# Kernel tuning notes

Measured on AMD Instinct MI355X. Metric: run time of the kernel, lower is better.

## Reference

```python
import jax, jax.numpy as jnp
import numpy as np

NUM_HEADS = 16


def _mhsa(x, Wq, Wk, Wv, Wo):
    B, S, D = x.shape
    H = NUM_HEADS
    dk = D // H
    # Linear applies weight [out, in]: y = x @ W.T
    Q = jnp.einsum('bsd,ed->bse', x, Wq).reshape(B, S, H, dk).transpose(0, 2, 1, 3)
    K = jnp.einsum('bsd,ed->bse', x, Wk).reshape(B, S, H, dk).transpose(0, 2, 1, 3)
    V = jnp.einsum('bsd,ed->bse', x, Wv).reshape(B, S, H, dk).transpose(0, 2, 1, 3)
    scores = jnp.einsum('bhqd,bhkd->bhqk', Q, K) / jnp.sqrt(jnp.asarray(dk, x.dtype))
    causal = jnp.tril(jnp.ones((S, S), dtype=bool))  # True = keep
    scores = jnp.where(causal, scores, jnp.asarray(-jnp.inf, x.dtype))
    attn = jax.nn.softmax(scores, axis=-1)
    out = jnp.einsum('bhqk,bhkd->bhqd', attn, V)  # [B,H,S,dk]
    out = out.transpose(0, 2, 1, 3).reshape(B, S, D)
    return jnp.einsum('bsd,ed->bse', out, Wo)


def setup_inputs() -> dict:
    key = jax.random.key(0)
    ks = jax.random.split(key, 5)
    B, S, D = 4, 2048, 1024
    std = 2.0 / (D + D) ** 0.5
    return {
        'x': jax.random.normal(ks[0], (B, S, D), dtype=jnp.float32),
        'Wq': jax.random.normal(ks[1], (D, D), dtype=jnp.float32) * std,
        'Wk': jax.random.normal(ks[2], (D, D), dtype=jnp.float32) * std,
        'Wv': jax.random.normal(ks[3], (D, D), dtype=jnp.float32) * std,
        'Wo': jax.random.normal(ks[4], (D, D), dtype=jnp.float32) * std,
    }


def reference(x, Wq, Wk, Wv, Wo):
    return _mhsa(x, Wq, Wk, Wv, Wo)
```

## Files before the change

### kernel.cpp

```cpp
#include <hip/hip_runtime.h>
#include <hip/hip_bf16.h>
#include <stdint.h>

typedef __attribute__((ext_vector_type(8))) short short8;
typedef __attribute__((ext_vector_type(4))) float f32x4;

static __device__ __forceinline__ void gload_lds16(const void* g, void* l) {
  __builtin_amdgcn_global_load_lds((const __attribute__((address_space(1))) void*)g,
                                   (__attribute__((address_space(3))) void*)l,
                                   16, 0, 0);
}

static __device__ __forceinline__ unsigned short f2bf(float f) {
  union { __hip_bfloat16 h; unsigned short s; } u;
  u.h = __float2bfloat16(f);
  return u.s;
}

__global__ void cast_all(const float* __restrict__ x, const float* __restrict__ Wq,
                         const float* __restrict__ Wk, const float* __restrict__ Wv,
                         const float* __restrict__ Wo,
                         unsigned short* __restrict__ xb, unsigned short* __restrict__ Wqb,
                         unsigned short* __restrict__ Wkb, unsigned short* __restrict__ Wvb,
                         unsigned short* __restrict__ Wob) {
  const int i = blockIdx.x * 256 + threadIdx.x;
  const float* src;
  unsigned short* dst;
  int off;
  if (i < 2097152) {
    src = x; dst = xb; off = i;
  } else {
    const int j = i - 2097152;
    const int wsel = j >> 18;
    off = j & 262143;
    src = wsel == 0 ? Wq : wsel == 1 ? Wk : wsel == 2 ? Wv : Wo;
    dst = wsel == 0 ? Wqb : wsel == 1 ? Wkb : wsel == 2 ? Wvb : Wob;
  }
  float4 v = reinterpret_cast<const float4*>(src)[off];
  ushort4 o;
  o.x = f2bf(v.x); o.y = f2bf(v.y); o.z = f2bf(v.z); o.w = f2bf(v.w);
  reinterpret_cast<ushort4*>(dst)[off] = o;
}

template <typename OutT>
static __device__ __forceinline__ void gemm_tile(const unsigned short* __restrict__ A,
                                                 const unsigned short* __restrict__ B,
                                                 OutT* __restrict__ C,
                                                 int brow, int bcol, int ldc,
                                                 short* sA0, short* sA1,
                                                 short* sB0, short* sB1) {
  const int t = threadIdx.x;
  const int w = t >> 6, l = t & 63, lg = l >> 4, lr = l & 15;
  const int wr = w >> 1, wc = w & 1;
  short* sAb[2] = {sA0, sA1};
  short* sBb[2] = {sB0, sB1};

  f32x4 acc[4][4] = {};

  auto stage = [&](int buf, int kt) {
#pragma unroll
    for (int r = 0; r < 2; ++r) {
      const int byteoff = t * 16 + r * 4096;
      const int row = byteoff >> 6, inrow = byteoff & 63;
      gload_lds16((const char*)A + ((size_t)(brow + row) * 1024 + kt) * 2 + inrow,
                  (char*)sAb[buf] + byteoff);
      gload_lds16((const char*)B + ((size_t)(bcol + row) * 1024 + kt) * 2 + inrow,
                  (char*)sBb[buf] + byteoff);
    }
  };

  stage(0, 0);
  __syncthreads();
  int cur = 0;

  for (int kti = 0; kti < 32; ++kti) {
    if (kti + 1 < 32) stage(cur ^ 1, (kti + 1) << 5);

    short8 af[4], bfr[4];
#pragma unroll
    for (int m = 0; m < 4; ++m)
      af[m] = *reinterpret_cast<const short8*>(sAb[cur] + (wr * 64 + m * 16 + lr) * 32 + lg * 8);
#pragma unroll
    for (int n = 0; n < 4; ++n)
      bfr[n] = *reinterpret_cast<const short8*>(sBb[cur] + (wc * 64 + n * 16 + lr) * 32 + lg * 8);
#pragma unroll
    for (int m = 0; m < 4; ++m)
#pragma unroll
      for (int n = 0; n < 4; ++n)
        acc[m][n] = __builtin_amdgcn_mfma_f32_16x16x32_bf16(af[m], bfr[n], acc[m][n], 0, 0, 0);

    __syncthreads();
    cur ^= 1;
  }

#pragma unroll
  for (int m = 0; m < 4; ++m) {
#pragma unroll
    for (int n = 0; n < 4; ++n) {
#pragma unroll
      for (int j = 0; j < 4; ++j) {
        const int rr = brow + wr * 64 + m * 16 + lg * 4 + j;
        const int cc = bcol + wc * 64 + n * 16 + lr;
        if constexpr (sizeof(OutT) == 2) {
          C[(size_t)rr * ldc + cc] = (OutT)f2bf(acc[m][n][j]);
        } else {
          C[(size_t)rr * ldc + cc] = acc[m][n][j];
        }
      }
    }
  }
}

__global__ __launch_bounds__(256) void gemm_qkv(const unsigned short* __restrict__ xb,
                                                const unsigned short* __restrict__ Wqb,
                                                const unsigned short* __restrict__ Wkb,
                                                const unsigned short* __restrict__ Wvb,
                                                unsigned short* __restrict__ Qb,
                                                unsigned short* __restrict__ Kb,
                                                unsigned short* __restrict__ Vt) {
  __shared__ short sA[2][4096];
  __shared__ short sB[2][4096];
  const int i = blockIdx.x;
  const int lid = (i & 7) * 192 + (i >> 3);
  const int z = lid >> 9, r = lid & 511;

  const unsigned short *A, *B;
  unsigned short* C;
  int brow, bcol, ldc;
  if (z == 2) {
    A = Wvb; B = xb; C = Vt;
    brow = (r & 7) << 7; bcol = (r >> 3) << 7; ldc = 8192;
  } else {
    A = xb; B = z ? Wkb : Wqb; C = z ? Kb : Qb;
    brow = (r >> 3) << 7; bcol = (r & 7) << 7; ldc = 1024;
  }
  gemm_tile<unsigned short>(A, B, C, brow, bcol, ldc, sA[0], sA[1], sB[0], sB[1]);
}

__global__ __launch_bounds__(256) void gemm_out(const unsigned short* __restrict__ AO,
                                                const unsigned short* __restrict__ Wob,
                                                float* __restrict__ out) {
  __shared__ short sA[2][4096];
  __shared__ short sB[2][4096];
  const int i = blockIdx.x;
  const int lid = (i & 7) * 64 + (i >> 3);
  gemm_tile<float>(AO, Wob, out, (lid >> 3) << 7, (lid & 7) << 7, 1024,
                   sA[0], sA[1], sB[0], sB[1]);
}

__global__ __launch_bounds__(256) void attn_kernel(const unsigned short* __restrict__ Qg,
                                                   const unsigned short* __restrict__ Kg,
                                                   const unsigned short* __restrict__ Vtg,
                                                   unsigned short* __restrict__ AO) {
  const int S = 2048, D = 1024, SN = 8192;
  const int i = blockIdx.x;
  const int lid = (i & 7) * 128 + (i >> 3);
  const int qp = lid & 15;
  const int bh = lid >> 4;
  const int b = bh >> 4, h = bh & 15;
  const int t = threadIdx.x;
  const int w = t >> 6, l = t & 63, lg = l >> 4, lr = l & 15;

  __shared__ short sK[2][64 * 64];
  __shared__ short sV[2][64 * 64];
  __shared__ short sP[4 * 16 * 64];

  int sboff[2], slin[2], srow[2];
#pragma unroll
  for (int r = 0; r < 2; ++r) {
    sboff[r] = t * 16 + r * 4096;
    srow[r] = sboff[r] >> 7;
    slin[r] = (sboff[r] & 127) ^ ((srow[r] & 7) << 4);
  }
  const char* Kbase = (const char*)Kg + ((size_t)(b * S) * D + h * 64) * 2;
  const char* Vbase = (const char*)Vtg + ((size_t)(h * 64) * SN + (size_t)b * S) * 2;

  auto stage = [&](int buf, int kvt) {
    const size_t kv0 = (size_t)kvt * 64;
#pragma unroll
    for (int r = 0; r < 2; ++r) {
      gload_lds16(Kbase + (kv0 + srow[r]) * 2048 + slin[r], (char*)sK[buf] + sboff[r]);
      gload_lds16(Vbase + (size_t)srow[r] * 16384 + kv0 * 2 + slin[r],
                  (char*)sV[buf] + sboff[r]);
    }
  };

  const float SCL = 0.125f * 1.44269504089f;
  int cur = 0;
  stage(0, 0);

#pragma unroll 1
  for (int half = 0; half < 2; ++half) {
    const int qt = half ? (31 - qp) : qp;
    const int nkv = qt + 1;

    short8 qf[2];
    {
      const unsigned short* qbase =
          Qg + (size_t)(b * S + qt * 64 + w * 16 + lr) * D + h * 64;
      qf[0] = *reinterpret_cast<const short8*>(qbase + lg * 8);
      qf[1] = *reinterpret_cast<const short8*>(qbase + 32 + lg * 8);
    }

    f32x4 o[4] = {};
    float m = -INFINITY, lsum = 0.f;

    __syncthreads();

    for (int kvt = 0; kvt < nkv; ++kvt) {
      if (kvt + 1 < nkv) stage(cur ^ 1, kvt + 1);

      const char* sKc = (const char*)sK[cur];
      const char* sVc = (const char*)sV[cur];

      f32x4 sc[4] = {};
      __builtin_amdgcn_s_setprio(1);
#pragma unroll
      for (int n = 0; n < 4; ++n) {
#pragma unroll
        for (int kk = 0; kk < 2; ++kk) {
          const int row = n * 16 + lr;
          const short8 kf = *reinterpret_cast<const short8*>(
              sKc + (row << 7) + ((kk * 64 + lg * 16) ^ ((row & 7) << 4)));
          sc[n] = __builtin_amdgcn_mfma_f32_16x16x32_bf16(kf, qf[kk], sc[n], 0, 0, 0);
        }
      }
      __builtin_amdgcn_s_setprio(0);

      float p[4][4];
      const bool diag = (kvt == qt);
      const int ql = w * 16 + lr;
#pragma unroll
      for (int n = 0; n < 4; ++n) {
#pragma unroll
        for (int r = 0; r < 4; ++r) {
          float v = sc[n][r] * SCL;
          if (diag && (n * 16 + lg * 4 + r) > ql) v = -INFINITY;
          p[n][r] = v;
        }
      }

      float mx = p[0][0];
#pragma unroll
      for (int n = 0; n < 4; ++n)
#pragma unroll
        for (int r = 0; r < 4; ++r) mx = fmaxf(mx, p[n][r]);
      mx = fmaxf(mx, __shfl_xor(mx, 16));
      mx = fmaxf(mx, __shfl_xor(mx, 32));
      if (!__all(mx <= m + 8.0f)) {
        const float mnew = fmaxf(m, mx);
        const float alpha = __builtin_amdgcn_exp2f(m - mnew);
        m = mnew;
        lsum *= alpha;
#pragma unroll
        for (int dn = 0; dn < 4; ++dn) o[dn] *= alpha;
      }

      float s = 0.f;
#pragma unroll
      for (int n = 0; n < 4; ++n) {
#pragma unroll
        for (int r = 0; r < 4; ++r) {
          const float e = __builtin_amdgcn_exp2f(p[n][r] - m);
          p[n][r] = e;
          s += e;
        }
      }
      s += __shfl_xor(s, 16);
      s += __shfl_xor(s, 32);
      lsum += s;

#pragma unroll
      for (int n = 0; n < 4; ++n) {
        ushort4 pk;
        pk.x = f2bf(p[n][0]); pk.y = f2bf(p[n][1]);
        pk.z = f2bf(p[n][2]); pk.w = f2bf(p[n][3]);
        *reinterpret_cast<ushort4*>(
            (char*)sP + (w << 11) + (lr << 7) + ((n * 32 + lg * 8) ^ ((lr & 7) << 4))) = pk;
      }

      __builtin_amdgcn_s_setprio(1);
#pragma unroll
      for (int kk = 0; kk < 2; ++kk) {
        const short8 pa = *reinterpret_cast<const short8*>(
            (const char*)sP + (w << 11) + (lr << 7) +
            ((kk * 64 + lg * 16) ^ ((lr & 7) << 4)));
#pragma unroll
        for (int dn = 0; dn < 4; ++dn) {
          const int vrow = dn * 16 + lr;
          const short8 vb = *reinterpret_cast<const short8*>(
              sVc + (vrow << 7) + ((kk * 64 + lg * 16) ^ ((vrow & 7) << 4)));
          o[dn] = __builtin_amdgcn_mfma_f32_16x16x32_bf16(vb, pa, o[dn], 0, 0, 0);
        }
      }
      __builtin_amdgcn_s_setprio(0);

      __syncthreads();
      cur ^= 1;
    }

    if (half == 0) stage(cur, 0);

    const float inv = 1.f / lsum;
    unsigned short* orow = AO + (size_t)(b * S + qt * 64 + w * 16 + lr) * D + h * 64;
#pragma unroll
    for (int dn = 0; dn < 4; ++dn) {
      ushort4 ov;
      ov.x = f2bf(o[dn][0] * inv); ov.y = f2bf(o[dn][1] * inv);
      ov.z = f2bf(o[dn][2] * inv); ov.w = f2bf(o[dn][3] * inv);
      *reinterpret_cast<ushort4*>(orow + dn * 16 + lg * 4) = ov;
    }
  }
}

extern "C" void kernel_launch(void* const* d_in, const int* in_sizes, int n_in,
                              void* d_out, int out_size, void* d_ws, size_t ws_size,
                              hipStream_t stream) {
  const float* x  = (const float*)d_in[0];
  const float* Wq = (const float*)d_in[1];
  const float* Wk = (const float*)d_in[2];
  const float* Wv = (const float*)d_in[3];
  const float* Wo = (const float*)d_in[4];
  float* out = (float*)d_out;

  char* ws = (char*)d_ws;
  unsigned short* xb  = (unsigned short*)(ws);
  unsigned short* Wqb = (unsigned short*)(ws + 16777216);
  unsigned short* Wkb = (unsigned short*)(ws + 18874368);
  unsigned short* Wvb = (unsigned short*)(ws + 20971520);
  unsigned short* Wob = (unsigned short*)(ws + 23068672);
  unsigned short* Qb  = (unsigned short*)(ws + 25165824);
  unsigned short* Kb  = (unsigned short*)(ws + 41943040);
  unsigned short* Vt  = (unsigned short*)(ws + 58720256);
  unsigned short* AO  = (unsigned short*)(ws + 75497472);

  cast_all<<<12288, 256, 0, stream>>>(x, Wq, Wk, Wv, Wo, xb, Wqb, Wkb, Wvb, Wob);
  gemm_qkv<<<1536, 256, 0, stream>>>(xb, Wqb, Wkb, Wvb, Qb, Kb, Vt);
  attn_kernel<<<1024, 256, 0, stream>>>(Qb, Kb, Vt, AO);
  gemm_out<<<512, 256, 0, stream>>>(AO, Wob, out);
}
```

Measured before the change: 286.1 us.

## Triple-buffer GEMM and attention loads with single barrier and swizzled LDS

GEMM tiles switch from double to triple LDS buffering, prefetch two stages ahead, and use a single waitcnt+barrier per iteration in place of two syncthreads. The GEMM LDS rows are XOR-swizzled to cut bank conflicts on the fragment reads. The attention kernel merges its two causal query-tile halves into one flat 33-step loop, so K/V prefetch runs across the half boundary without a pipeline drain. The cost is more LDS per block, which may lower occupancy, and reliance on hand-written vmcnt counts being correct.

```diff
diff --git a/kernel.cpp b/kernel.cpp
--- a/kernel.cpp
+++ b/kernel.cpp
@@ -16,6 +16,9 @@
   u.h = __float2bfloat16(f);
   return u.s;
 }
+
+#define WAIT4_BARRIER() asm volatile("s_waitcnt vmcnt(4) lgkmcnt(0)\n\ts_barrier" ::: "memory")
+#define WAIT0_BARRIER() asm volatile("s_waitcnt vmcnt(0) lgkmcnt(0)\n\ts_barrier" ::: "memory")
 
 __global__ void cast_all(const float* __restrict__ x, const float* __restrict__ Wq,
                          const float* __restrict__ Wk, const float* __restrict__ Wv,
@@ -47,13 +50,10 @@
                                                  const unsigned short* __restrict__ B,
                                                  OutT* __restrict__ C,
                                                  int brow, int bcol, int ldc,
-                                                 short* sA0, short* sA1,
-                                                 short* sB0, short* sB1) {
+                                                 short* sA, short* sB) {
   const int t = threadIdx.x;
   const int w = t >> 6, l = t & 63, lg = l >> 4, lr = l & 15;
   const int wr = w >> 1, wc = w & 1;
-  short* sAb[2] = {sA0, sA1};
-  short* sBb[2] = {sB0, sB1};
 
   f32x4 acc[4][4] = {};
 
@@ -61,36 +61,51 @@
 #pragma unroll
     for (int r = 0; r < 2; ++r) {
       const int byteoff = t * 16 + r * 4096;
-      const int row = byteoff >> 6, inrow = byteoff & 63;
+      const int row = byteoff >> 6;
+      const int inrow = (byteoff & 63) ^ (((row >> 1) & 3) << 4);
       gload_lds16((const char*)A + ((size_t)(brow + row) * 1024 + kt) * 2 + inrow,
-                  (char*)sAb[buf] + byteoff);
+                  (char*)(sA + buf * 4096) + byteoff);
       gload_lds16((const char*)B + ((size_t)(bcol + row) * 1024 + kt) * 2 + inrow,
-                  (char*)sBb[buf] + byteoff);
+                  (char*)(sB + buf * 4096) + byteoff);
     }
   };
 
   stage(0, 0);
-  __syncthreads();
+  stage(1, 32);
   int cur = 0;
 
   for (int kti = 0; kti < 32; ++kti) {
-    if (kti + 1 < 32) stage(cur ^ 1, (kti + 1) << 5);
+    if (kti < 31) WAIT4_BARRIER();
+    else         WAIT0_BARRIER();
+    if (kti + 2 < 32) {
+      int b2 = cur + 2; if (b2 >= 3) b2 -= 3;
+      stage(b2, (kti + 2) << 5);
+    }
+    const char* sAc = (const char*)(sA + cur * 4096);
+    const char* sBc = (const char*)(sB + cur * 4096);
 
     short8 af[4], bfr[4];
 #pragma unroll
-    for (int m = 0; m < 4; ++m)
-      af[m] = *reinterpret_cast<const short8*>(sAb[cur] + (wr * 64 + m * 16 + lr) * 32 + lg * 8);
-#pragma unroll
-    for (int n = 0; n < 4; ++n)
-      bfr[n] = *reinterpret_cast<const short8*>(sBb[cur] + (wc * 64 + n * 16 + lr) * 32 + lg * 8);
+    for (int m = 0; m < 4; ++m) {
+      const int arow = wr * 64 + m * 16 + lr;
+      af[m] = *reinterpret_cast<const short8*>(
+          sAc + arow * 64 + ((lg * 16) ^ (((arow >> 1) & 3) << 4)));
+    }
+#pragma unroll
+    for (int n = 0; n < 4; ++n) {
+      const int brw = wc * 64 + n * 16 + lr;
+      bfr[n] = *reinterpret_cast<const short8*>(
+          sBc + brw * 64 + ((lg * 16) ^ (((brw >> 1) & 3) << 4)));
+    }
+    __builtin_amdgcn_s_setprio(1);
 #pragma unroll
     for (int m = 0; m < 4; ++m)
 #pragma unroll
       for (int n = 0; n < 4; ++n)
         acc[m][n] = __builtin_amdgcn_mfma_f32_16x16x32_bf16(af[m], bfr[n], acc[m][n], 0, 0, 0);
-
-    __syncthreads();
-    cur ^= 1;
+    __builtin_amdgcn_s_setprio(0);
+
+    ++cur; if (cur == 3) cur = 0;
   }
 
 #pragma unroll
@@ -118,8 +133,8 @@
                                                 unsigned short* __restrict__ Qb,
                                                 unsigned short* __restrict__ Kb,
                                                 unsigned short* __restrict__ Vt) {
-  __shared__ short sA[2][4096];
-  __shared__ short sB[2][4096];
+  __shared__ short sA[3][4096];
+  __shared__ short sB[3][4096];
   const int i = blockIdx.x;
   const int lid = (i & 7) * 192 + (i >> 3);
   const int z = lid >> 9, r = lid & 511;
@@ -134,18 +149,17 @@
     A = xb; B = z ? Wkb : Wqb; C = z ? Kb : Qb;
     brow = (r >> 3) << 7; bcol = (r & 7) << 7; ldc = 1024;
   }
-  gemm_tile<unsigned short>(A, B, C, brow, bcol, ldc, sA[0], sA[1], sB[0], sB[1]);
+  gemm_tile<unsigned short>(A, B, C, brow, bcol, ldc, sA[0], sB[0]);
 }
 
 __global__ __launch_bounds__(256) void gemm_out(const unsigned short* __restrict__ AO,
                                                 const unsigned short* __restrict__ Wob,
                                                 float* __restrict__ out) {
-  __shared__ short sA[2][4096];
-  __shared__ short sB[2][4096];
+  __shared__ short sA[3][4096];
+  __shared__ short sB[3][4096];
   const int i = blockIdx.x;
   const int lid = (i & 7) * 64 + (i >> 3);
-  gemm_tile<float>(AO, Wob, out, (lid >> 3) << 7, (lid & 7) << 7, 1024,
-                   sA[0], sA[1], sB[0], sB[1]);
+  gemm_tile<float>(AO, Wob, out, (lid >> 3) << 7, (lid & 7) << 7, 1024, sA[0], sB[0]);
 }
 
 __global__ __launch_bounds__(256) void attn_kernel(const unsigned short* __restrict__ Qg,
@@ -161,9 +175,9 @@
   const int t = threadIdx.x;
   const int w = t >> 6, l = t & 63, lg = l >> 4, lr = l & 15;
 
-  __shared__ short sK[2][64 * 64];
-  __shared__ short sV[2][64 * 64];
-  __shared__ short sP[4 * 16 * 64];
+  __shared__ short sK[3][4096];
+  __shared__ short sV[3][4096];
+  __shared__ short sP[4096];
 
   int sboff[2], slin[2], srow[2];
 #pragma unroll
@@ -175,132 +189,39 @@
   const char* Kbase = (const char*)Kg + ((size_t)(b * S) * D + h * 64) * 2;
   const char* Vbase = (const char*)Vtg + ((size_t)(h * 64) * SN + (size_t)b * S) * 2;
 
-  auto stage = [&](int buf, int kvt) {
+  const int nkv0 = qp + 1;
+  const int qt1 = 31 - qp;
+
+  auto stage = [&](int buf, int j) {
+    const int kvt = (j < nkv0) ? j : j - nkv0;
     const size_t kv0 = (size_t)kvt * 64;
 #pragma unroll
     for (int r = 0; r < 2; ++r) {
-      gload_lds16(Kbase + (kv0 + srow[r]) * 2048 + slin[r], (char*)sK[buf] + sboff[r]);
+      gload_lds16(Kbase + (kv0 + srow[r]) * 2048 + slin[r],
+                  (char*)sK + buf * 8192 + sboff[r]);
       gload_lds16(Vbase + (size_t)srow[r] * 16384 + kv0 * 2 + slin[r],
-                  (char*)sV[buf] + sboff[r]);
+                  (char*)sV + buf * 8192 + sboff[r]);
     }
   };
+  auto load_qf = [&](int qt, short8* qf) {
+    const unsigned short* qbase =
+        Qg + (size_t)(b * S + qt * 64 + w * 16 + lr) * D + h * 64;
+    qf[0] = *reinterpret_cast<const short8*>(qbase + lg * 8);
+    qf[1] = *reinterpret_cast<const short8*>(qbase + 32 + lg * 8);
+  };
 
   const float SCL = 0.125f * 1.44269504089f;
+
+  short8 qf[2];
+  load_qf(qp, qf);
+  stage(0, 0);
+  stage(1, 1);
+
+  f32x4 o[4] = {};
+  float m = -INFINITY, lsum = 0.f;
   int cur = 0;
-  stage(0, 0);
-
-#pragma unroll 1
-  for (int half = 0; half < 2; ++half) {
-    const int qt = half ? (31 - qp) : qp;
-    const int nkv = qt + 1;
-
-    short8 qf[2];
-    {
-      const unsigned short* qbase =
-          Qg + (size_t)(b * S + qt * 64 + w * 16 + lr) * D + h * 64;
-      qf[0] = *reinterpret_cast<const short8*>(qbase + lg * 8);
-      qf[1] = *reinterpret_cast<const short8*>(qbase + 32 + lg * 8);
-    }
-
-    f32x4 o[4] = {};
-    float m = -INFINITY, lsum = 0.f;
-
-    __syncthreads();
-
-    for (int kvt = 0; kvt < nkv; ++kvt) {
-      if (kvt + 1 < nkv) stage(cur ^ 1, kvt + 1);
-
-      const char* sKc = (const char*)sK[cur];
-      const char* sVc = (const char*)sV[cur];
-
-      f32x4 sc[4] = {};
-      __builtin_amdgcn_s_setprio(1);
-#pragma unroll
-      for (int n = 0; n < 4; ++n) {
-#pragma unroll
-        for (int kk = 0; kk < 2; ++kk) {
-          const int row = n * 16 + lr;
-          const short8 kf = *reinterpret_cast<const short8*>(
-              sKc + (row << 7) + ((kk * 64 + lg * 16) ^ ((row & 7) << 4)));
-          sc[n] = __builtin_amdgcn_mfma_f32_16x16x32_bf16(kf, qf[kk], sc[n], 0, 0, 0);
-        }
-      }
-      __builtin_amdgcn_s_setprio(0);
-
-      float p[4][4];
-      const bool diag = (kvt == qt);
-      const int ql = w * 16 + lr;
-#pragma unroll
-      for (int n = 0; n < 4; ++n) {
-#pragma unroll
-        for (int r = 0; r < 4; ++r) {
-          float v = sc[n][r] * SCL;
-          if (diag && (n * 16 + lg * 4 + r) > ql) v = -INFINITY;
-          p[n][r] = v;
-        }
-      }
-
-      float mx = p[0][0];
-#pragma unroll
-      for (int n = 0; n < 4; ++n)
-#pragma unroll
-        for (int r = 0; r < 4; ++r) mx = fmaxf(mx, p[n][r]);
-      mx = fmaxf(mx, __shfl_xor(mx, 16));
-      mx = fmaxf(mx, __shfl_xor(mx, 32));
-      if (!__all(mx <= m + 8.0f)) {
-        const float mnew = fmaxf(m, mx);
-        const float alpha = __builtin_amdgcn_exp2f(m - mnew);
-        m = mnew;
-        lsum *= alpha;
-#pragma unroll
-        for (int dn = 0; dn < 4; ++dn) o[dn] *= alpha;
-      }
-
-      float s = 0.f;
-#pragma unroll
-      for (int n = 0; n < 4; ++n) {
-#pragma unroll
-        for (int r = 0; r < 4; ++r) {
-          const float e = __builtin_amdgcn_exp2f(p[n][r] - m);
-          p[n][r] = e;
-          s += e;
-        }
-      }
-      s += __shfl_xor(s, 16);
-      s += __shfl_xor(s, 32);
-      lsum += s;
-
-#pragma unroll
-      for (int n = 0; n < 4; ++n) {
-        ushort4 pk;
-        pk.x = f2bf(p[n][0]); pk.y = f2bf(p[n][1]);
-        pk.z = f2bf(p[n][2]); pk.w = f2bf(p[n][3]);
-        *reinterpret_cast<ushort4*>(
-            (char*)sP + (w << 11) + (lr << 7) + ((n * 32 + lg * 8) ^ ((lr & 7) << 4))) = pk;
-      }
-
-      __builtin_amdgcn_s_setprio(1);
-#pragma unroll
-      for (int kk = 0; kk < 2; ++kk) {
-        const short8 pa = *reinterpret_cast<const short8*>(
-            (const char*)sP + (w << 11) + (lr << 7) +
-            ((kk * 64 + lg * 16) ^ ((lr & 7) << 4)));
-#pragma unroll
-        for (int dn = 0; dn < 4; ++dn) {
-          const int vrow = dn * 16 + lr;
-          const short8 vb = *reinterpret_cast<const short8*>(
-              sVc + (vrow << 7) + ((kk * 64 + lg * 16) ^ ((vrow & 7) << 4)));
-          o[dn] = __builtin_amdgcn_mfma_f32_16x16x32_bf16(vb, pa, o[dn], 0, 0, 0);
-        }
-      }
-      __builtin_amdgcn_s_setprio(0);
-
-      __syncthreads();
-      cur ^= 1;
-    }
-
-    if (half == 0) stage(cur, 0);
-
+
+  auto epilogue = [&](int qt) {
     const float inv = 1.f / lsum;
     unsigned short* orow = AO + (size_t)(b * S + qt * 64 + w * 16 + lr) * D + h * 64;
 #pragma unroll
@@ -310,7 +231,117 @@
       ov.z = f2bf(o[dn][2] * inv); ov.w = f2bf(o[dn][3] * inv);
       *reinterpret_cast<ushort4*>(orow + dn * 16 + lg * 4) = ov;
     }
-  }
+  };
+
+#pragma unroll 1
+  for (int j = 0; j < 33; ++j) {
+    const bool h1 = (j >= nkv0);
+    const int kvt = h1 ? j - nkv0 : j;
+    const int qt = h1 ? qt1 : qp;
+
+    if (j < 32) WAIT4_BARRIER();
+    else        WAIT0_BARRIER();
+    if (j + 2 < 33) {
+      int b2 = cur + 2; if (b2 >= 3) b2 -= 3;
+      stage(b2, j + 2);
+    }
+
+    const char* sKc = (const char*)sK + cur * 8192;
+    const char* sVc = (const char*)sV + cur * 8192;
+
+    f32x4 sc[4] = {};
+    __builtin_amdgcn_s_setprio(1);
+#pragma unroll
+    for (int n = 0; n < 4; ++n) {
+#pragma unroll
+      for (int kk = 0; kk < 2; ++kk) {
+        const int row = n * 16 + lr;
+        const short8 kf = *reinterpret_cast<const short8*>(
+            sKc + (row << 7) + ((kk * 64 + lg * 16) ^ ((row & 7) << 4)));
+        sc[n] = __builtin_amdgcn_mfma_f32_16x16x32_bf16(kf, qf[kk], sc[n], 0, 0, 0);
+      }
+    }
+    __builtin_amdgcn_s_setprio(0);
+
+    float p[4][4];
+    const bool diag = (kvt == qt);
+    const int ql = w * 16 + lr;
+#pragma unroll
+    for (int n = 0; n < 4; ++n) {
+#pragma unroll
+      for (int r = 0; r < 4; ++r) {
+        float v = sc[n][r] * SCL;
+        if (diag && (n * 16 + lg * 4 + r) > ql) v = -INFINITY;
+        p[n][r] = v;
+      }
+    }
+
+    float mx = p[0][0];
+#pragma unroll
+    for (int n = 0; n < 4; ++n)
+#pragma unroll
+      for (int r = 0; r < 4; ++r) mx = fmaxf(mx, p[n][r]);
+    mx = fmaxf(mx, __shfl_xor(mx, 16));
+    mx = fmaxf(mx, __shfl_xor(mx, 32));
+    if (!__all(mx <= m + 8.0f)) {
+      const float mnew = fmaxf(m, mx);
+      const float alpha = __builtin_amdgcn_exp2f(m - mnew);
+      m = mnew;
+      lsum *= alpha;
+#pragma unroll
+      for (int dn = 0; dn < 4; ++dn) o[dn] *= alpha;
+    }
+
+    float s = 0.f;
+#pragma unroll
+    for (int n = 0; n < 4; ++n) {
+#pragma unroll
+      for (int r = 0; r < 4; ++r) {
+        const float e = __builtin_amdgcn_exp2f(p[n][r] - m);
+        p[n][r] = e;
+        s += e;
+      }
+    }
+    s += __shfl_xor(s, 16);
+    s += __shfl_xor(s, 32);
+    lsum += s;
+
+#pragma unroll
+    for (int n = 0; n < 4; ++n) {
+      ushort4 pk;
+      pk.x = f2bf(p[n][0]); pk.y = f2bf(p[n][1]);
+      pk.z = f2bf(p[n][2]); pk.w = f2bf(p[n][3]);
+      *reinterpret_cast<ushort4*>(
+          (char*)sP + (w << 11) + (lr << 7) + ((n * 32 + lg * 8) ^ ((lr & 7) << 4))) = pk;
+    }
+
+    __builtin_amdgcn_s_setprio(1);
+#pragma unroll
+    for (int kk = 0; kk < 2; ++kk) {
+      const short8 pa = *reinterpret_cast<const short8*>(
+          (const char*)sP + (w << 11) + (lr << 7) +
+          ((kk * 64 + lg * 16) ^ ((lr & 7) << 4)));
+#pragma unroll
+      for (int dn = 0; dn < 4; ++dn) {
+        const int vrow = dn * 16 + lr;
+        const short8 vb = *reinterpret_cast<const short8*>(
+            sVc + (vrow << 7) + ((kk * 64 + lg * 16) ^ ((vrow & 7) << 4)));
+        o[dn] = __builtin_amdgcn_mfma_f32_16x16x32_bf16(vb, pa, o[dn], 0, 0, 0);
+      }
+    }
+    __builtin_amdgcn_s_setprio(0);
+
+    if (j == nkv0 - 1) {
+      epilogue(qp);
+#pragma unroll
+      for (int dn = 0; dn < 4; ++dn) o[dn] = f32x4{0.f, 0.f, 0.f, 0.f};
+      m = -INFINITY; lsum = 0.f;
+      load_qf(qt1, qf);
+    }
+
+    ++cur; if (cur == 3) cur = 0;
+  }
+  epilogue(qt1);
 }
 
 extern "C" void kernel_launch(void* const* d_in, const int* in_sizes, int n_in,
```

Measured after the change: 274.0 us. 4.2% less time.
